# Performance work log

Hardware: AMD Instinct MI355X
Metric: run time of the kernel (lower is better)

## Reference

```python
import jax, jax.numpy as jnp
import numpy as np

EPS = 1e-5


def conv3x3(x, w, b):
    # x [B,C,H,W], w [O,C,3,3], stride 1, pad 1
    y = jax.lax.conv_general_dilated(x, w, (1, 1), ((1, 1), (1, 1)),
                                     dimension_numbers=('NCHW', 'OIHW', 'NCHW'))
    return y + b[None, :, None, None]


def bilinear_gather(x, py, px):
    # x [B,C,H,W]; sampling locations py,px [B,K,H,W] -> [B,C,K,H,W]
    # Zero padding outside the image (matches deform_conv CUDA semantics:
    # out-of-bound corner values contribute 0).
    B, C, H, W = x.shape
    K = py.shape[1]
    x_flat = x.reshape(B, C, H * W)
    y0 = jnp.floor(py)
    x0 = jnp.floor(px)
    out = jnp.zeros((B, C, K, H, W), x.dtype)
    for dy in (0.0, 1.0):
        for dx in (0.0, 1.0):
            yi = y0 + dy
            xi = x0 + dx
            wgt = (1.0 - jnp.abs(py - yi)) * (1.0 - jnp.abs(px - xi))  # [B,K,H,W]
            valid = (yi >= 0) & (yi <= H - 1) & (xi >= 0) & (xi <= W - 1)
            idx = (jnp.clip(yi, 0, H - 1).astype(jnp.int32) * W
                   + jnp.clip(xi, 0, W - 1).astype(jnp.int32)).reshape(B, -1)
            vals = jax.vmap(lambda xf, i: xf[:, i])(x_flat, idx)  # [B,C,K*H*W]
            out = out + (wgt * valid)[:, None] * vals.reshape(B, C, K, H, W)
    return out


def setup_inputs() -> dict:
    key = jax.random.key(0)
    k1, k2, k3 = jax.random.split(key, 3)
    B, C, O, H, W = 4, 64, 64, 128, 128
    x = jax.random.normal(k1, (B, C, H, W), jnp.float32)
    # offset predictor: small init so predicted offsets are modest (realistic)
    off_w = 0.01 * jax.random.normal(k2, (18, C, 3, 3), jnp.float32)
    off_b = jnp.zeros((18,), jnp.float32)
    dc_w = jax.random.normal(k3, (O, C, 3, 3), jnp.float32) / np.sqrt(C * 9)
    dc_b = jnp.zeros((O,), jnp.float32)
    gamma = jnp.ones((O,), jnp.float32)
    beta = jnp.zeros((O,), jnp.float32)
    return {"x": x, "off_w": off_w, "off_b": off_b, "dc_w": dc_w,
            "dc_b": dc_b, "gamma": gamma, "beta": beta}


def reference(x, off_w, off_b, dc_w, dc_b, gamma, beta):
    B, C, H, W = x.shape
    O = dc_w.shape[0]
    K = 9  # 3x3 kernel
    offset = conv3x3(x, off_w, off_b)              # [B,18,H,W]
    off = offset.reshape(B, K, 2, H, W)            # (dy,dx) per kernel tap, row-major
    dyo, dxo = off[:, :, 0], off[:, :, 1]          # [B,K,H,W]
    k = (jnp.arange(3) - 1).astype(x.dtype)        # kernel taps {-1,0,1}
    kgy = jnp.repeat(k, 3)                         # [9] row-major y offsets
    kgx = jnp.tile(k, 3)                           # [9] row-major x offsets
    hh = jnp.arange(H, dtype=x.dtype)
    ww = jnp.arange(W, dtype=x.dtype)
    # stride 1, pad 1: base point = out_pos - 1 + tap; pad is folded into kgy/kgx
    py = hh[None, None, :, None] + kgy[None, :, None, None] + dyo
    px = ww[None, None, None, :] + kgx[None, :, None, None] + dxo
    sampled = bilinear_gather(x, py, px)           # [B,C,K,H,W]
    y = jnp.einsum('ock,bckhw->bohw', dc_w.reshape(O, C, K), sampled)
    y = y + dc_b[None, :, None, None]
    # BatchNorm2d (training mode: biased batch statistics)
    mu = y.mean(axis=(0, 2, 3), keepdims=True)
    var = y.var(axis=(0, 2, 3), keepdims=True)
    yn = (y - mu) * jax.lax.rsqrt(var + EPS)
    return jax.nn.relu(yn * gamma[None, :, None, None] + beta[None, :, None, None])
```

## Files before the change

kernel.cpp:

```cpp
#include <hip/hip_runtime.h>

#define HH 128
#define WW 128
#define HWSZ (HH * WW)
#define CC 64
#define OO 64
#define BB 4
#define NOFF 18
#define KK 576

#define WS_BG     0
#define WS_BGO    18432
#define WS_SUMS   27648
#define WS_SUMSQ  27712
#define WS_YBUF   27776

typedef __attribute__((ext_vector_type(8))) short short8;
typedef __attribute__((ext_vector_type(4))) int int4v;
typedef __attribute__((ext_vector_type(4))) float f32x4;

__device__ inline unsigned bf16rne(float f) {
  unsigned u = __float_as_uint(f);
  u += 0x7fff + ((u >> 16) & 1);
  return u >> 16;
}

__global__ __launch_bounds__(256) void prep_kernel(
    const float* __restrict__ x, const float* __restrict__ off_w,
    const float* __restrict__ dc_w, unsigned int* __restrict__ xTu,
    int* __restrict__ Bg, int* __restrict__ Bgo, float* __restrict__ sums) {
  int bid = blockIdx.x;
  if (bid < BB * HH) {
    __shared__ float T[CC][WW + 1];
    int b = bid >> 7, h = bid & 127;
    int tw = threadIdx.x & 127, th = threadIdx.x >> 7;
    const float* xp = x + (size_t)b * CC * HWSZ + h * WW;
#pragma unroll 8
    for (int i = 0; i < 32; ++i) {
      int c = i * 2 + th;
      T[c][tw] = xp[c * HWSZ + tw];
    }
    __syncthreads();
    int c2 = threadIdx.x & 31, wq = threadIdx.x >> 5;
    unsigned int* op = xTu + ((size_t)(b * HH + h) * WW) * 32;
#pragma unroll 8
    for (int i = 0; i < 16; ++i) {
      int w = i * 8 + wq;
      unsigned pk = bf16rne(T[2 * c2][w]) | (bf16rne(T[2 * c2 + 1][w]) << 16);
      op[w * 32 + c2] = pk;
    }
  } else {
    int pb = bid - BB * HH;
    int tid = pb * 256 + threadIdx.x;
    int stride = 64 * 256;
    for (int i = tid; i < 72 * 64 * 4; i += stride) {
      int j = i & 3, o = (i >> 2) & 63, g = i >> 8;
      int k2 = g * 4 + j, t = k2 >> 5, jj = k2 & 31;
      unsigned lo = bf16rne(dc_w[o * KK + (2 * jj) * 9 + t]);
      unsigned hi = bf16rne(dc_w[o * KK + (2 * jj + 1) * 9 + t]);
      Bg[i] = (int)(lo | (hi << 16));
    }
    for (int i = tid; i < 72 * 32 * 4; i += stride) {
      int j = i & 3, o = (i >> 2) & 31, g = i >> 7;
      int k2 = g * 4 + j, t = k2 >> 5, jj = k2 & 31;
      unsigned pk = 0;
      if (o < NOFF) {
        unsigned lo = bf16rne(off_w[o * KK + (2 * jj) * 9 + t]);
        unsigned hi = bf16rne(off_w[o * KK + (2 * jj + 1) * 9 + t]);
        pk = lo | (hi << 16);
      }
      Bgo[i] = (int)pk;
    }
    if (tid < 128) sums[tid] = 0.0f;
  }
}

#define G_ISSUE(i, TAP, PH)                                                   \
  int4v m##i, da##i, db##i, dcv##i, dd##i;                                    \
  {                                                                           \
    m##i = *(const int4v*)&Mw[(((PH) * 8 + p8) * 9 + (TAP)) * 4];             \
    unsigned x_ = (unsigned)m##i.x, y_ = (unsigned)m##i.y;                    \
    da##i  = *(const int4v*)&xbu[(x_ & 0xffffu) * 32 + cq4];                  \
    db##i  = *(const int4v*)&xbu[(x_ >> 16) * 32 + cq4];                      \
    dcv##i = *(const int4v*)&xbu[(y_ & 0xffffu) * 32 + cq4];                  \
    dd##i  = *(const int4v*)&xbu[(y_ >> 16) * 32 + cq4];                      \
  }

#define G_BLEND(i, TL, PH)                                                    \
  {                                                                           \
    int pxl_ = (PH) * 8 + p8;                                                 \
    float w00_ = __uint_as_float(((unsigned)m##i.z) << 16);                   \
    float w01_ = __uint_as_float(((unsigned)m##i.z) & 0xffff0000u);           \
    float w10_ = __uint_as_float(((unsigned)m##i.w) << 16);                   \
    float w11_ = __uint_as_float(((unsigned)m##i.w) & 0xffff0000u);           \
    int4v pk_;                                                                \
    _Pragma("unroll")                                                         \
    for (int j = 0; j < 4; ++j) {                                             \
      float slo_ = w00_ * __uint_as_float(((unsigned)da##i[j]) << 16);        \
      slo_ = fmaf(w01_, __uint_as_float(((unsigned)db##i[j]) << 16), slo_);   \
      slo_ = fmaf(w10_, __uint_as_float(((unsigned)dcv##i[j]) << 16), slo_);  \
      slo_ = fmaf(w11_, __uint_as_float(((unsigned)dd##i[j]) << 16), slo_);   \
      float shi_ = w00_ * __uint_as_float(((unsigned)da##i[j]) & 0xffff0000u);\
      shi_ = fmaf(w01_, __uint_as_float(((unsigned)db##i[j]) & 0xffff0000u), shi_);\
      shi_ = fmaf(w10_, __uint_as_float(((unsigned)dcv##i[j]) & 0xffff0000u), shi_);\
      shi_ = fmaf(w11_, __uint_as_float(((unsigned)dd##i[j]) & 0xffff0000u), shi_);\
      pk_[j] = (int)__builtin_amdgcn_perm(__float_as_uint(shi_) + 0x8000u,    \
                                          __float_as_uint(slo_) + 0x8000u,    \
                                          0x07060302u);                       \
    }                                                                         \
    *(int4v*)&A[(p0 + pxl_) * 100 + (TL) * 32 + cq4] = pk_;                   \
  }

__global__ __launch_bounds__(256, 4) void fused_kernel(
    const unsigned int* __restrict__ xTu, const int* __restrict__ Bg,
    const int* __restrict__ Bgo, const float* __restrict__ off_b,
    const float* __restrict__ dc_b, float* __restrict__ ybuf,
    float* __restrict__ part) {
  __shared__ __align__(16) int A[4 * 16 * 100];
  __shared__ __align__(16) int M[4 * 144 * 4];
  __shared__ float offL[4][NOFF][16];

  int cg = threadIdx.x >> 6, lane = threadIdx.x & 63;
  int b = blockIdx.x >> 8, rem = blockIdx.x & 255;
  int h = rem >> 1, w0 = (rem & 1) * 64;
  int hw0 = h * WW + w0;
  int p0 = cg * 16;
  int n16 = lane & 15, q = lane >> 4;
  int pg = lane >> 3, part8 = lane & 7;
  const unsigned int* xbu = xTu + (size_t)b * HWSZ * 32;

  f32x4 acc2[2] = {f32x4{0, 0, 0, 0}, f32x4{0, 0, 0, 0}};
#pragma unroll 1
  for (int chunk = 0; chunk < 3; ++chunk) {
    int cy = h + chunk - 1;
    bool vy = (cy >= 0) && (cy < HH);
    int cys = min(max(cy, 0), HH - 1);
#pragma unroll
    for (int tl = 0; tl < 3; ++tl) {
#pragma unroll
      for (int i = 0; i < 2; ++i) {
        int px = i * 8 + pg;
        int cx = w0 + p0 + px + tl - 1;
        bool v = vy && (cx >= 0) && (cx < WW);
        int cxs = min(max(cx, 0), WW - 1);
        int4v val = *(const int4v*)&xbu[(cys * WW + cxs) * 32 + part8 * 4];
        if (!v) { val.x = 0; val.y = 0; val.z = 0; val.w = 0; }
        *(int4v*)&A[(p0 + px) * 100 + tl * 32 + part8 * 4] = val;
      }
    }
#pragma unroll 2
    for (int kk = 0; kk < 6; ++kk) {
      int4v av = *(const int4v*)&A[(p0 + n16) * 100 + kk * 16 + q * 4];
      short8 af = __builtin_bit_cast(short8, av);
      int g = chunk * 24 + kk * 4 + q;
#pragma unroll
      for (int nt = 0; nt < 2; ++nt) {
        int4v bv = *(const int4v*)&Bgo[(g * 32 + nt * 16 + n16) * 4];
        short8 bfr = __builtin_bit_cast(short8, bv);
        acc2[nt] = __builtin_amdgcn_mfma_f32_16x16x32_bf16(af, bfr, acc2[nt], 0, 0, 0);
      }
    }
  }
#pragma unroll
  for (int nt = 0; nt < 2; ++nt) {
    int o = nt * 16 + n16;
    if (o < NOFF) {
      float bv = off_b[o];
#pragma unroll
      for (int r = 0; r < 4; ++r) offL[cg][o][q * 4 + r] = acc2[nt][r] + bv;
    }
  }

  int* Mw = M + cg * 144 * 4;
#pragma unroll
  for (int it = 0; it < 3; ++it) {
    int m = it * 64 + lane;
    if (m < 144) {
      int pxl = (unsigned)m / 9u;
      int t = m - pxl * 9;
      float dy = offL[cg][2 * t][pxl];
      float dx = offL[cg][2 * t + 1][pxl];
      float py = (float)(h + t / 3 - 1) + dy;
      float pxf = (float)(w0 + p0 + pxl + (t % 3) - 1) + dx;
      float fy0 = floorf(py), fx0 = floorf(pxf);
      float ay = py - fy0, ax = pxf - fx0;
      int iy0 = (int)fy0, ix0 = (int)fx0;
      int iy1 = iy0 + 1, ix1 = ix0 + 1;
      float wy0 = 1.0f - ay, wy1 = ay, wx0 = 1.0f - ax, wx1 = ax;
      if (!(iy0 >= 0 && iy0 < HH)) wy0 = 0.0f;
      if (!(iy1 >= 0 && iy1 < HH)) wy1 = 0.0f;
      if (!(ix0 >= 0 && ix0 < WW)) wx0 = 0.0f;
      if (!(ix1 >= 0 && ix1 < WW)) wx1 = 0.0f;
      int cy0 = min(max(iy0, 0), HH - 1), cy1 = min(max(iy1, 0), HH - 1);
      int cx0 = min(max(ix0, 0), WW - 1), cx1 = min(max(ix1, 0), WW - 1);
      int4v mv;
      mv.x = (cy0 * WW + cx0) | ((cy0 * WW + cx1) << 16);
      mv.y = (cy1 * WW + cx0) | ((cy1 * WW + cx1) << 16);
      mv.z = (int)(bf16rne(wy0 * wx0) | (bf16rne(wy0 * wx1) << 16));
      mv.w = (int)(bf16rne(wy1 * wx0) | (bf16rne(wy1 * wx1) << 16));
      *(int4v*)&Mw[m * 4] = mv;
    }
  }

  int p8 = lane >> 3;
  int cq4 = (lane & 7) * 4;
  f32x4 acc[4] = {f32x4{0,0,0,0}, f32x4{0,0,0,0}, f32x4{0,0,0,0}, f32x4{0,0,0,0}};
#pragma unroll 1
  for (int chunk = 0; chunk < 3; ++chunk) {
    int tap0 = chunk * 3;
    G_ISSUE(0, tap0 + 0, 0)
    G_ISSUE(1, tap0 + 0, 1)
    G_ISSUE(2, tap0 + 1, 0)
    G_BLEND(0, 0, 0)
    G_ISSUE(3, tap0 + 1, 1)
    G_BLEND(1, 0, 1)
    G_ISSUE(4, tap0 + 2, 0)
    G_BLEND(2, 1, 0)
    G_ISSUE(5, tap0 + 2, 1)
    G_BLEND(3, 1, 1)
    G_BLEND(4, 2, 0)
    G_BLEND(5, 2, 1)
#pragma unroll 2
    for (int kk = 0; kk < 6; ++kk) {
      int4v av = *(const int4v*)&A[(p0 + n16) * 100 + kk * 16 + q * 4];
      short8 af = __builtin_bit_cast(short8, av);
      int g = chunk * 24 + kk * 4 + q;
#pragma unroll
      for (int nt = 0; nt < 4; ++nt) {
        int4v bv = *(const int4v*)&Bg[(g * 64 + nt * 16 + n16) * 4];
        short8 bfr = __builtin_bit_cast(short8, bv);
        acc[nt] = __builtin_amdgcn_mfma_f32_16x16x32_bf16(af, bfr, acc[nt], 0, 0, 0);
      }
    }
  }

  float* SW = (float*)&A[cg * 1600];
#pragma unroll
  for (int nt = 0; nt < 4; ++nt) {
    int o = nt * 16 + n16;
    float bv = dc_b[o];
    f32x4 r;
    float s = 0.0f, ss = 0.0f;
#pragma unroll
    for (int r0 = 0; r0 < 4; ++r0) {
      r[r0] = acc[nt][r0] + bv;
      s += r[r0];
      ss += r[r0] * r[r0];
    }
    *(f32x4*)(ybuf + (size_t)(b * OO + o) * HWSZ + hw0 + p0 + q * 4) = r;
    s += __shfl_xor(s, 16);  s += __shfl_xor(s, 32);
    ss += __shfl_xor(ss, 16); ss += __shfl_xor(ss, 32);
    if (lane < 16) {
      SW[nt * 16 + lane] = s;
      SW[64 + nt * 16 + lane] = ss;
    }
  }
  __syncthreads();
  if (threadIdx.x < 64) {
    float ts = 0.0f, tq = 0.0f;
#pragma unroll
    for (int wv = 0; wv < 4; ++wv) {
      const float* Sv = (const float*)&A[wv * 1600];
      ts += Sv[threadIdx.x];
      tq += Sv[64 + threadIdx.x];
    }
    part[(size_t)blockIdx.x * 128 + threadIdx.x] = ts;
    part[(size_t)blockIdx.x * 128 + 64 + threadIdx.x] = tq;
  }
}

__global__ __launch_bounds__(64) void reduce_kernel(
    const float* __restrict__ part, float* __restrict__ sums) {
  int t = blockIdx.x;
  int j = threadIdx.x;
  float s = 0.0f;
#pragma unroll
  for (int k = 0; k < 16; ++k) s += part[(size_t)(j + 64 * k) * 128 + t];
#pragma unroll
  for (int off = 32; off > 0; off >>= 1) s += __shfl_down(s, off);
  if (j == 0) sums[t] = s;
}

__global__ __launch_bounds__(256) void norm_kernel(
    const float* __restrict__ ybuf, const float* __restrict__ sums,
    const float* __restrict__ sumsq, const float* __restrict__ gamma,
    const float* __restrict__ beta, float* __restrict__ out) {
  int gid = blockIdx.x * 256 + threadIdx.x;
  int flat = gid << 2;
  int o = (flat >> 14) & 63;
  const float invN = 1.0f / (float)(BB * HWSZ);
  float mean = sums[o] * invN;
  float var = sumsq[o] * invN - mean * mean;
  float rstd = rsqrtf(var + 1e-5f);
  float g = gamma[o] * rstd;
  float bta = beta[o] - mean * g;
  float4 v = ((const float4*)ybuf)[gid];
  float4 r;
  r.x = fmaxf(v.x * g + bta, 0.0f);
  r.y = fmaxf(v.y * g + bta, 0.0f);
  r.z = fmaxf(v.z * g + bta, 0.0f);
  r.w = fmaxf(v.w * g + bta, 0.0f);
  ((float4*)out)[gid] = r;
}

extern "C" void kernel_launch(void* const* d_in, const int* in_sizes, int n_in,
                              void* d_out, int out_size, void* d_ws, size_t ws_size,
                              hipStream_t stream) {
  const float* x     = (const float*)d_in[0];
  const float* off_w = (const float*)d_in[1];
  const float* off_b = (const float*)d_in[2];
  const float* dc_w  = (const float*)d_in[3];
  const float* dc_b  = (const float*)d_in[4];
  const float* gamma = (const float*)d_in[5];
  const float* beta  = (const float*)d_in[6];
  float* ws = (float*)d_ws;
  int*   Bg     = (int*)(ws + WS_BG);
  int*   Bgo    = (int*)(ws + WS_BGO);
  float* sums   = ws + WS_SUMS;
  float* sumsq  = ws + WS_SUMSQ;
  float* ybuf   = ws + WS_YBUF;
  float* out = (float*)d_out;
  unsigned int* xTu = (unsigned int*)d_out;
  float* part = (float*)d_out + 2097152;

  prep_kernel<<<BB * HH + 64, 256, 0, stream>>>(x, off_w, dc_w, xTu, Bg, Bgo, sums);
  fused_kernel<<<BB * HWSZ / 64, 256, 0, stream>>>(xTu, Bg, Bgo, off_b, dc_b, ybuf, part);
  reduce_kernel<<<128, 64, 0, stream>>>(part, sums);
  norm_kernel<<<BB * OO * HWSZ / (4 * 256), 256, 0, stream>>>(ybuf, sums, sumsq, gamma, beta, out);
}
```

Baseline: 125.5 us.

## Pipeline per-tap gather with MFMA, shrink LDS, store pre-BN output in bf16

Restructures the deformable gather and GEMM loop into a per-tap software pipeline. Gathers for tap t+1 are issued while tap t is blended and fed to MFMAs, using a double-buffered LDS tile of 34-int rows instead of a 3-tap chunk buffer. Freeing LDS (offL reuses A) lets occupancy rise from 4 to 6 blocks per CU. The intermediate conv output is now stored as bf16 and expanded in the norm kernel, which halves that round trip's memory traffic at some cost in precision.

```diff
diff --git a/kernel.cpp b/kernel.cpp
--- a/kernel.cpp
+++ b/kernel.cpp
@@ -17,6 +17,7 @@
 
 typedef __attribute__((ext_vector_type(8))) short short8;
 typedef __attribute__((ext_vector_type(4))) int int4v;
+typedef __attribute__((ext_vector_type(2))) unsigned int uint2v;
 typedef __attribute__((ext_vector_type(4))) float f32x4;
 
 __device__ inline unsigned bf16rne(float f) {
@@ -75,10 +76,10 @@
   }
 }
 
-#define G_ISSUE(i, TAP, PH)                                                   \
+#define G_ISSUE(i, T, PH)                                                     \
   int4v m##i, da##i, db##i, dcv##i, dd##i;                                    \
   {                                                                           \
-    m##i = *(const int4v*)&Mw[(((PH) * 8 + p8) * 9 + (TAP)) * 4];             \
+    m##i = *(const int4v*)&Mw[(((PH) * 8 + p8) * 9 + (T)) * 4];               \
     unsigned x_ = (unsigned)m##i.x, y_ = (unsigned)m##i.y;                    \
     da##i  = *(const int4v*)&xbu[(x_ & 0xffffu) * 32 + cq4];                  \
     db##i  = *(const int4v*)&xbu[(x_ >> 16) * 32 + cq4];                      \
@@ -86,9 +87,8 @@
     dd##i  = *(const int4v*)&xbu[(y_ >> 16) * 32 + cq4];                      \
   }
 
-#define G_BLEND(i, TL, PH)                                                    \
+#define G_BLEND(i, T, PH)                                                     \
   {                                                                           \
-    int pxl_ = (PH) * 8 + p8;                                                 \
     float w00_ = __uint_as_float(((unsigned)m##i.z) << 16);                   \
     float w01_ = __uint_as_float(((unsigned)m##i.z) & 0xffff0000u);           \
     float w10_ = __uint_as_float(((unsigned)m##i.w) << 16);                   \
@@ -108,51 +108,66 @@
                                           __float_as_uint(slo_) + 0x8000u,    \
                                           0x07060302u);                       \
     }                                                                         \
-    *(int4v*)&A[(p0 + pxl_) * 100 + (TL) * 32 + cq4] = pk_;                   \
-  }
-
-__global__ __launch_bounds__(256, 4) void fused_kernel(
+    *(int4v*)&A[abase + ((T) & 1) * 544 + ((PH) * 8 + p8) * 34 + cq4] = pk_;  \
+  }
+
+#define MFMA_TAP(T)                                                           \
+  {                                                                           \
+    _Pragma("unroll")                                                         \
+    for (int kk2 = 0; kk2 < 2; ++kk2) {                                       \
+      int4v av = *(const int4v*)&A[abase + ((T) & 1) * 544 + n16 * 34 + kk2 * 16 + q * 4]; \
+      short8 af = __builtin_bit_cast(short8, av);                             \
+      int g = (T) * 8 + kk2 * 4 + q;                                          \
+      _Pragma("unroll")                                                       \
+      for (int nt = 0; nt < 4; ++nt) {                                        \
+        int4v bv = *(const int4v*)&Bg[(g * 64 + nt * 16 + n16) * 4];          \
+        short8 bfr = __builtin_bit_cast(short8, bv);                          \
+        acc[nt] = __builtin_amdgcn_mfma_f32_16x16x32_bf16(af, bfr, acc[nt], 0, 0, 0); \
+      }                                                                       \
+    }                                                                         \
+  }
+
+__global__ __launch_bounds__(256, 6) void fused_kernel(
     const unsigned int* __restrict__ xTu, const int* __restrict__ Bg,
     const int* __restrict__ Bgo, const float* __restrict__ off_b,
-    const float* __restrict__ dc_b, float* __restrict__ ybuf,
+    const float* __restrict__ dc_b, unsigned int* __restrict__ ybuf,
     float* __restrict__ part) {
-  __shared__ __align__(16) int A[4 * 16 * 100];
+  __shared__ __align__(16) int A[4 * 1088];
   __shared__ __align__(16) int M[4 * 144 * 4];
-  __shared__ float offL[4][NOFF][16];
 
   int cg = threadIdx.x >> 6, lane = threadIdx.x & 63;
   int b = blockIdx.x >> 8, rem = blockIdx.x & 255;
   int h = rem >> 1, w0 = (rem & 1) * 64;
   int hw0 = h * WW + w0;
   int p0 = cg * 16;
+  int abase = cg * 1088;
   int n16 = lane & 15, q = lane >> 4;
   int pg = lane >> 3, part8 = lane & 7;
   const unsigned int* xbu = xTu + (size_t)b * HWSZ * 32;
 
   f32x4 acc2[2] = {f32x4{0, 0, 0, 0}, f32x4{0, 0, 0, 0}};
-#pragma unroll 1
-  for (int chunk = 0; chunk < 3; ++chunk) {
-    int cy = h + chunk - 1;
+#pragma unroll
+  for (int t = 0; t < 9; ++t) {
+    int ky = t / 3 - 1, kx = t % 3 - 1;
+    int cy = h + ky;
     bool vy = (cy >= 0) && (cy < HH);
     int cys = min(max(cy, 0), HH - 1);
-#pragma unroll
-    for (int tl = 0; tl < 3; ++tl) {
-#pragma unroll
-      for (int i = 0; i < 2; ++i) {
-        int px = i * 8 + pg;
-        int cx = w0 + p0 + px + tl - 1;
-        bool v = vy && (cx >= 0) && (cx < WW);
-        int cxs = min(max(cx, 0), WW - 1);
-        int4v val = *(const int4v*)&xbu[(cys * WW + cxs) * 32 + part8 * 4];
-        if (!v) { val.x = 0; val.y = 0; val.z = 0; val.w = 0; }
-        *(int4v*)&A[(p0 + px) * 100 + tl * 32 + part8 * 4] = val;
-      }
-    }
-#pragma unroll 2
-    for (int kk = 0; kk < 6; ++kk) {
-      int4v av = *(const int4v*)&A[(p0 + n16) * 100 + kk * 16 + q * 4];
+    int tb = abase + (t & 1) * 544;
+#pragma unroll
+    for (int i = 0; i < 2; ++i) {
+      int px = i * 8 + pg;
+      int cx = w0 + p0 + px + kx;
+      bool v = vy && (cx >= 0) && (cx < WW);
+      int cxs = min(max(cx, 0), WW - 1);
+      int4v val = *(const int4v*)&xbu[(cys * WW + cxs) * 32 + part8 * 4];
+      if (!v) { val.x = 0; val.y = 0; val.z = 0; val.w = 0; }
+      *(int4v*)&A[tb + px * 34 + part8 * 4] = val;
+    }
+#pragma unroll
+    for (int kk2 = 0; kk2 < 2; ++kk2) {
+      int4v av = *(const int4v*)&A[tb + n16 * 34 + kk2 * 16 + q * 4];
       short8 af = __builtin_bit_cast(short8, av);
-      int g = chunk * 24 + kk * 4 + q;
+      int g = t * 8 + kk2 * 4 + q;
 #pragma unroll
       for (int nt = 0; nt < 2; ++nt) {
         int4v bv = *(const int4v*)&Bgo[(g * 32 + nt * 16 + n16) * 4];
@@ -161,13 +176,14 @@
       }
     }
   }
+  float* offLw = (float*)&A[abase];
 #pragma unroll
   for (int nt = 0; nt < 2; ++nt) {
     int o = nt * 16 + n16;
     if (o < NOFF) {
       float bv = off_b[o];
 #pragma unroll
-      for (int r = 0; r < 4; ++r) offL[cg][o][q * 4 + r] = acc2[nt][r] + bv;
+      for (int r = 0; r < 4; ++r) offLw[o * 16 + q * 4 + r] = acc2[nt][r] + bv;
     }
   }
 
@@ -178,8 +194,8 @@
     if (m < 144) {
       int pxl = (unsigned)m / 9u;
       int t = m - pxl * 9;
-      float dy = offL[cg][2 * t][pxl];
-      float dx = offL[cg][2 * t + 1][pxl];
+      float dy = offLw[(2 * t) * 16 + pxl];
+      float dx = offLw[(2 * t + 1) * 16 + pxl];
       float py = (float)(h + t / 3 - 1) + dy;
       float pxf = (float)(w0 + p0 + pxl + (t % 3) - 1) + dx;
       float fy0 = floorf(py), fx0 = floorf(pxf);
@@ -205,36 +221,18 @@
   int p8 = lane >> 3;
   int cq4 = (lane & 7) * 4;
   f32x4 acc[4] = {f32x4{0,0,0,0}, f32x4{0,0,0,0}, f32x4{0,0,0,0}, f32x4{0,0,0,0}};
-#pragma unroll 1
-  for (int chunk = 0; chunk < 3; ++chunk) {
-    int tap0 = chunk * 3;
-    G_ISSUE(0, tap0 + 0, 0)
-    G_ISSUE(1, tap0 + 0, 1)
-    G_ISSUE(2, tap0 + 1, 0)
-    G_BLEND(0, 0, 0)
-    G_ISSUE(3, tap0 + 1, 1)
-    G_BLEND(1, 0, 1)
-    G_ISSUE(4, tap0 + 2, 0)
-    G_BLEND(2, 1, 0)
-    G_ISSUE(5, tap0 + 2, 1)
-    G_BLEND(3, 1, 1)
-    G_BLEND(4, 2, 0)
-    G_BLEND(5, 2, 1)
-#pragma unroll 2
-    for (int kk = 0; kk < 6; ++kk) {
-      int4v av = *(const int4v*)&A[(p0 + n16) * 100 + kk * 16 + q * 4];
-      short8 af = __builtin_bit_cast(short8, av);
-      int g = chunk * 24 + kk * 4 + q;
-#pragma unroll
-      for (int nt = 0; nt < 4; ++nt) {
-        int4v bv = *(const int4v*)&Bg[(g * 64 + nt * 16 + n16) * 4];
-        short8 bfr = __builtin_bit_cast(short8, bv);
-        acc[nt] = __builtin_amdgcn_mfma_f32_16x16x32_bf16(af, bfr, acc[nt], 0, 0, 0);
-      }
-    }
-  }
-
-  float* SW = (float*)&A[cg * 1600];
+  G_ISSUE(0, 0, 0)   G_ISSUE(1, 0, 1)
+  G_ISSUE(2, 1, 0)   G_ISSUE(3, 1, 1)   G_BLEND(0, 0, 0)   G_BLEND(1, 0, 1)   MFMA_TAP(0)
+  G_ISSUE(4, 2, 0)   G_ISSUE(5, 2, 1)   G_BLEND(2, 1, 0)   G_BLEND(3, 1, 1)   MFMA_TAP(1)
+  G_ISSUE(6, 3, 0)   G_ISSUE(7, 3, 1)   G_BLEND(4, 2, 0)   G_BLEND(5, 2, 1)   MFMA_TAP(2)
+  G_ISSUE(8, 4, 0)   G_ISSUE(9, 4, 1)   G_BLEND(6, 3, 0)   G_BLEND(7, 3, 1)   MFMA_TAP(3)
+  G_ISSUE(10, 5, 0)  G_ISSUE(11, 5, 1)  G_BLEND(8, 4, 0)   G_BLEND(9, 4, 1)   MFMA_TAP(4)
+  G_ISSUE(12, 6, 0)  G_ISSUE(13, 6, 1)  G_BLEND(10, 5, 0)  G_BLEND(11, 5, 1)  MFMA_TAP(5)
+  G_ISSUE(14, 7, 0)  G_ISSUE(15, 7, 1)  G_BLEND(12, 6, 0)  G_BLEND(13, 6, 1)  MFMA_TAP(6)
+  G_ISSUE(16, 8, 0)  G_ISSUE(17, 8, 1)  G_BLEND(14, 7, 0)  G_BLEND(15, 7, 1)  MFMA_TAP(7)
+  G_BLEND(16, 8, 0)  G_BLEND(17, 8, 1)  MFMA_TAP(8)
+
+  float* SW = (float*)&A[abase];
 #pragma unroll
   for (int nt = 0; nt < 4; ++nt) {
     int o = nt * 16 + n16;
@@ -247,7 +245,14 @@
       s += r[r0];
       ss += r[r0] * r[r0];
     }
-    *(f32x4*)(ybuf + (size_t)(b * OO + o) * HWSZ + hw0 + p0 + q * 4) = r;
+    unsigned pk0 = __builtin_amdgcn_perm(__float_as_uint(r[1]) + 0x8000u,
+                                         __float_as_uint(r[0]) + 0x8000u,
+                                         0x07060302u);
+    unsigned pk1 = __builtin_amdgcn_perm(__float_as_uint(r[3]) + 0x8000u,
+                                         __float_as_uint(r[2]) + 0x8000u,
+                                         0x07060302u);
+    uint2v pk; pk.x = pk0; pk.y = pk1;
+    *(uint2v*)&ybuf[(size_t)(b * OO + o) * (HWSZ / 2) + ((hw0 + p0) >> 1) + q * 2] = pk;
     s += __shfl_xor(s, 16);  s += __shfl_xor(s, 32);
     ss += __shfl_xor(ss, 16); ss += __shfl_xor(ss, 32);
     if (lane < 16) {
@@ -260,7 +265,7 @@
     float ts = 0.0f, tq = 0.0f;
 #pragma unroll
     for (int wv = 0; wv < 4; ++wv) {
-      const float* Sv = (const float*)&A[wv * 1600];
+      const float* Sv = (const float*)&A[wv * 1088];
       ts += Sv[threadIdx.x];
       tq += Sv[64 + threadIdx.x];
     }
@@ -282,7 +287,7 @@
 }
 
 __global__ __launch_bounds__(256) void norm_kernel(
-    const float* __restrict__ ybuf, const float* __restrict__ sums,
+    const unsigned int* __restrict__ ybuf, const float* __restrict__ sums,
     const float* __restrict__ sumsq, const float* __restrict__ gamma,
     const float* __restrict__ beta, float* __restrict__ out) {
   int gid = blockIdx.x * 256 + threadIdx.x;
@@ -294,12 +299,12 @@
   float rstd = rsqrtf(var + 1e-5f);
   float g = gamma[o] * rstd;
   float bta = beta[o] - mean * g;
-  float4 v = ((const float4*)ybuf)[gid];
+  uint2v v = ((const uint2v*)ybuf)[gid];
   float4 r;
-  r.x = fmaxf(v.x * g + bta, 0.0f);
-  r.y = fmaxf(v.y * g + bta, 0.0f);
-  r.z = fmaxf(v.z * g + bta, 0.0f);
-  r.w = fmaxf(v.w * g + bta, 0.0f);
+  r.x = fmaxf(__uint_as_float(v.x << 16) * g + bta, 0.0f);
+  r.y = fmaxf(__uint_as_float(v.x & 0xffff0000u) * g + bta, 0.0f);
+  r.z = fmaxf(__uint_as_float(v.y << 16) * g + bta, 0.0f);
+  r.w = fmaxf(__uint_as_float(v.y & 0xffff0000u) * g + bta, 0.0f);
   ((float4*)out)[gid] = r;
 }
 
@@ -318,7 +323,7 @@
   int*   Bgo    = (int*)(ws + WS_BGO);
   float* sums   = ws + WS_SUMS;
   float* sumsq  = ws + WS_SUMSQ;
-  float* ybuf   = ws + WS_YBUF;
+  unsigned int* ybuf = (unsigned int*)(ws + WS_YBUF);
   float* out = (float*)d_out;
   unsigned int* xTu = (unsigned int*)d_out;
   float* part = (float*)d_out + 2097152;
```

After: 125.3 us. Within noise of the previous version (-0.1%).
